# Performance work log

Measured on AMD Instinct MI355X. Metric: run time of the kernel, lower is better.

The kernel has to match this reference:

```python
import jax, jax.numpy as jnp
import numpy as np

NUM_EXPERTS = 8
TOP_K = 2
HIDDEN = 2048
FFN = 4096


def setup_inputs() -> dict:
    key = jax.random.key(0)
    ks = jax.random.split(key, 5)
    s = 0.02
    return {
        "hidden_states": jax.random.normal(ks[0], (2, 2048, HIDDEN), dtype=jnp.float32),
        "w_router": jax.random.normal(ks[1], (HIDDEN, NUM_EXPERTS), dtype=jnp.float32) * s,
        "w1": jax.random.normal(ks[2], (NUM_EXPERTS, FFN, HIDDEN), dtype=jnp.float32) * s,
        "w2": jax.random.normal(ks[3], (NUM_EXPERTS, HIDDEN, FFN), dtype=jnp.float32) * s,
        "w3": jax.random.normal(ks[4], (NUM_EXPERTS, FFN, HIDDEN), dtype=jnp.float32) * s,
    }


def reference(hidden_states, w_router, w1, w2, w3):
    shape = hidden_states.shape
    x = hidden_states.reshape(-1, HIDDEN)  # [T, H]

    # Router: logits -> softmax -> top-k -> renormalize (Mixtral routing)
    logits = x @ w_router                              # [T, E]
    probs = jax.nn.softmax(logits, axis=-1)
    top_w, top_i = jax.lax.top_k(probs, TOP_K)         # [T, K]
    top_w = top_w / jnp.sum(top_w, axis=-1, keepdims=True)
    # Dense combine weights per expert: [T, E]
    combine = jnp.sum(
        jax.nn.one_hot(top_i, NUM_EXPERTS, dtype=x.dtype) * top_w[..., None], axis=1
    )

    # Grouped SwiGLU experts: out = sum_e combine[:, e] * w2_e(silu(w1_e x) * w3_e x)
    out = jnp.zeros_like(x)
    for e in range(NUM_EXPERTS):
        h = jax.nn.silu(x @ w1[e].T) * (x @ w3[e].T)   # [T, F]
        y = h @ w2[e].T                                # [T, H]
        out = out + combine[:, e:e + 1] * y

    return (out.reshape(shape), jnp.zeros((1,), dtype=x.dtype))
```

## Files before the change

### kernel.cpp

```cpp
#include <hip/hip_runtime.h>
#include <hip/hip_bf16.h>
#include <stdint.h>

#define T_TOK 4096
#define HID   2048
#define FFN_D 4096
#define NE    8
#define PADB  256
#define PADMAX 10240

typedef __attribute__((ext_vector_type(8))) short  short8;
typedef __attribute__((ext_vector_type(4))) float  f32x4;
typedef __attribute__((ext_vector_type(4))) unsigned short u16x4;
typedef unsigned short u16;

__device__ __forceinline__ u16 f2bf(float f) {
    unsigned u = __float_as_uint(f);
    u += 0x7FFFu + ((u >> 16) & 1u);
    return (u16)(u >> 16);
}
__device__ __forceinline__ float bf2f(u16 v) {
    return __uint_as_float(((unsigned)v) << 16);
}

#define GLD16(g, l) __builtin_amdgcn_global_load_lds( \
    (const __attribute__((address_space(1))) unsigned int*)(g), \
    (__attribute__((address_space(3))) unsigned int*)(l), 16, 0, 0)

__global__ void k_convert(const float* __restrict__ s, u16* __restrict__ d, long n8) {
    for (long i = (long)blockIdx.x * 256 + threadIdx.x; i < n8; i += (long)gridDim.x * 256) {
        f32x4 a = *((const f32x4*)s + i * 2);
        f32x4 b = *((const f32x4*)s + i * 2 + 1);
        short8 o;
#pragma unroll
        for (int q = 0; q < 4; ++q) { o[q] = (short)f2bf(a[q]); o[q + 4] = (short)f2bf(b[q]); }
        *(short8*)(d + i * 8) = o;
    }
}

__global__ void k_convert2(const float* __restrict__ s0, u16* __restrict__ d0,
                           const float* __restrict__ s1, u16* __restrict__ d1, long n8) {
    for (long i = (long)blockIdx.x * 256 + threadIdx.x; i < 2 * n8; i += (long)gridDim.x * 256) {
        const float* s = (i < n8) ? s0 : s1;
        u16*         d = (i < n8) ? d0 : d1;
        long         j = (i < n8) ? i : (i - n8);
        f32x4 a = *((const f32x4*)s + j * 2);
        f32x4 b = *((const f32x4*)s + j * 2 + 1);
        short8 o;
#pragma unroll
        for (int q = 0; q < 4; ++q) { o[q] = (short)f2bf(a[q]); o[q + 4] = (short)f2bf(b[q]); }
        *(short8*)(d + j * 8) = o;
    }
}

__device__ __forceinline__ void router_body(
    int blk, int tid,
    const float* __restrict__ x, const float* __restrict__ wr,
    u16* __restrict__ xb, int* __restrict__ topk_id,
    float* __restrict__ topk_w, int* __restrict__ counts) {
    int lane = tid & 63;
    int t = blk * 4 + (tid >> 6);
    const float* xr = x + (size_t)t * HID;
    u16* xbr = xb + (size_t)t * HID;
    float acc[8];
#pragma unroll
    for (int e = 0; e < 8; ++e) acc[e] = 0.f;
    for (int h = lane; h < HID; h += 64) {
        float xv = xr[h];
        xbr[h] = f2bf(xv);
        f32x4 w0 = *(const f32x4*)(wr + h * 8);
        f32x4 w1 = *(const f32x4*)(wr + h * 8 + 4);
#pragma unroll
        for (int q = 0; q < 4; ++q) { acc[q] += xv * w0[q]; acc[4 + q] += xv * w1[q]; }
    }
#pragma unroll
    for (int e = 0; e < 8; ++e) {
        float v = acc[e];
#pragma unroll
        for (int s = 32; s > 0; s >>= 1) v += __shfl_xor(v, s);
        acc[e] = v;
    }
    if (lane == 0) {
        int i0 = 0; float l0 = acc[0];
#pragma unroll
        for (int e = 1; e < 8; ++e) if (acc[e] > l0) { l0 = acc[e]; i0 = e; }
        int i1 = -1; float l1 = -3.4e38f;
#pragma unroll
        for (int e = 0; e < 8; ++e) if (e != i0 && acc[e] > l1) { l1 = acc[e]; i1 = e; }
        float wA = 1.f / (1.f + expf(l1 - l0));
        topk_id[t * 2] = i0;  topk_id[t * 2 + 1] = i1;
        topk_w[t * 2] = wA;   topk_w[t * 2 + 1] = 1.f - wA;
        atomicAdd(&counts[i0], 1);
        atomicAdd(&counts[i1], 1);
    }
}

__global__ void k_router(const float* __restrict__ x, const float* __restrict__ wr,
                         u16* __restrict__ xb, int* __restrict__ topk_id,
                         float* __restrict__ topk_w, int* __restrict__ counts) {
    router_body(blockIdx.x, threadIdx.x, x, wr, xb, topk_id, topk_w, counts);
}

__global__ void k_pre(const float* __restrict__ x, const float* __restrict__ wr,
                      u16* __restrict__ xb, int* __restrict__ topk_id,
                      float* __restrict__ topk_w, int* __restrict__ counts,
                      const float* __restrict__ w1, u16* __restrict__ w1b,
                      const float* __restrict__ w3, u16* __restrict__ w3b, long n8) {
    if (blockIdx.x < 1024) {
        router_body(blockIdx.x, threadIdx.x, x, wr, xb, topk_id, topk_w, counts);
        return;
    }
    const long nb = (long)(gridDim.x - 1024);
    for (long i = (long)(blockIdx.x - 1024) * 256 + threadIdx.x; i < 2 * n8; i += nb * 256) {
        const float* s = (i < n8) ? w1 : w3;
        u16*         d = (i < n8) ? w1b : w3b;
        long         j = (i < n8) ? i : (i - n8);
        f32x4 a = *((const f32x4*)s + j * 2);
        f32x4 b = *((const f32x4*)s + j * 2 + 1);
        short8 o;
#pragma unroll
        for (int q = 0; q < 4; ++q) { o[q] = (short)f2bf(a[q]); o[q + 4] = (short)f2bf(b[q]); }
        *(short8*)(d + j * 8) = o;
    }
}

__global__ void k_scan(const int* __restrict__ counts, int* __restrict__ pad_off,
                       int* __restrict__ perm_tok) {
    __shared__ int sTot;
    if (threadIdx.x == 0) {
        int o = 0;
#pragma unroll
        for (int e = 0; e < 8; ++e) { pad_off[e] = o; o += ((counts[e] + PADB - 1) / PADB) * PADB; }
        pad_off[8] = o; sTot = o;
    }
    __syncthreads();
    int tot = sTot;
    for (int i = threadIdx.x; i < tot; i += 256) perm_tok[i] = 0;
}

__global__ void k_scatter(const int* __restrict__ topk_id, int* __restrict__ cursors,
                          const int* __restrict__ pad_off, int* __restrict__ perm_tok,
                          int* __restrict__ pos_of) {
    int t = blockIdx.x * 256 + threadIdx.x;
    if (t >= T_TOK) return;
#pragma unroll
    for (int k = 0; k < 2; ++k) {
        int e = topk_id[t * 2 + k];
        int p = pad_off[e] + atomicAdd(&cursors[e], 1);
        perm_tok[p] = t;
        pos_of[t * 2 + k] = p;
    }
}

template<int KTOT, int NTOT, int BNt, int KSPLIT, bool DUAL, bool GATHER, bool CONV>
__global__ __launch_bounds__(512, 2) void k_gemm8(
    const u16* __restrict__ A,
    const u16* __restrict__ B0all,
    const u16* __restrict__ B1all,
    u16* __restrict__ C,
    const int* __restrict__ perm_tok,
    const int* __restrict__ pad_off,
    const float* __restrict__ W2c,
    u16* __restrict__ W2d,
    int gemmBlk, int convBlk)
{
    constexpr int BMt   = 256;
    constexpr int WCW   = BNt / 4;
    constexpr int NI    = WCW / 16;
    constexpr int CPX   = (NTOT / BNt) / 8;
    constexpr int KPART = KTOT / KSPLIT;
    constexpr int NK    = KPART / 64;
    constexpr int ATILE = BMt * 64;
    constexpr int BTILE = BNt * 64;
    constexpr int SEGB  = DUAL ? 8 : (BNt == 256 ? 8 : 4);

    const int bid = blockIdx.x;
    const int tid = threadIdx.x;

    if (CONV && bid >= gemmBlk) {
        const long per = (long)NE * FFN_D * HID / 8 / convBlk;
        const long i0 = (long)(bid - gemmBlk) * per;
        for (long i = i0 + tid; i < i0 + per; i += 512) {
            f32x4 a = *((const f32x4*)W2c + i * 2);
            f32x4 b = *((const f32x4*)W2c + i * 2 + 1);
            short8 o;
#pragma unroll
            for (int q = 0; q < 4; ++q) { o[q] = (short)f2bf(a[q]); o[q + 4] = (short)f2bf(b[q]); }
            *(short8*)(W2d + i * 8) = o;
        }
        return;
    }

    const int xcd = bid & 7;
    int idx = bid >> 3;
    const int kh  = idx & (KSPLIT - 1);
    idx /= KSPLIT;
    const int m0  = (idx / CPX) * BMt;
    if (m0 >= pad_off[8]) return;
    const int n0  = (xcd * CPX + (idx % CPX)) * BNt;
    int e = 0;
    while (pad_off[e + 1] <= m0) ++e;

    __shared__ u16 As[2 * ATILE];
    __shared__ u16 Bs0[2 * BTILE];
    __shared__ u16 Bs1[DUAL ? 2 * BTILE : 8];
    __shared__ int tokS[GATHER ? BMt : 8];

    const int w = tid >> 6, l = tid & 63;
    if (GATHER) {
        for (int i = tid; i < BMt; i += 512) tokS[i] = perm_tok[m0 + i];
        __syncthreads();
    }

    const u16* B0 = B0all + (size_t)e * NTOT * KTOT;
    const u16* B1 = DUAL ? (B1all + (size_t)e * NTOT * KTOT) : B0all;
    const int k0e = kh * KPART;

    const int nseg = (w < 4) ? 8 : SEGB;
    const u16* gsrc[8];
    u16* ldst[8];
    int tstep;
    {
        const int c = (l & 7) ^ (l >> 3);
#pragma unroll
        for (int j = 0; j < 8; ++j) {
            const int js = (j < nseg) ? j : (j - 4);
            const int rl = js * 8 + (l >> 3);
            if (w < 4) {
                const int rt = w * 64 + rl;
                const long grow = GATHER ? (long)tokS[rt] : (long)(m0 + rt);
                gsrc[j] = A + grow * KTOT + k0e + c * 8;
                ldst[j] = (u16*)As + (w * 64 + js * 8) * 64;
                tstep = ATILE;
            } else if (DUAL && w >= 6) {
                const int rt = (w - 6) * 64 + rl;
                gsrc[j] = B1 + (size_t)(n0 + rt) * KTOT + k0e + c * 8;
                ldst[j] = (u16*)Bs1 + (rt - rl + js * 8) * 64;
                tstep = BTILE;
            } else {
                const int rt = DUAL ? ((w - 4) * 64 + rl)
                                    : (BNt == 256 ? ((w - 4) * 64 + rl)
                                                  : ((w - 4) * 32 + rl));
                gsrc[j] = B0 + (size_t)(n0 + rt) * KTOT + k0e + c * 8;
                ldst[j] = (u16*)Bs0 + (rt - rl + js * 8) * 64;
                tstep = BTILE;
            }
        }
    }

    const int wr = w >> 2, wc = w & 3;
    const int fr = l & 15, fk = l >> 4, x7 = l & 7;
    const int pc0 = ((fk ^ x7) << 3);
    const int pc1 = pc0 ^ 32;
    const int aB = (wr * 128 + fr) * 64;
    const int bB = (wc * WCW + fr) * 64;

    f32x4 acc0[8][NI], acc1[8][NI];
    const f32x4 fz = {0.f, 0.f, 0.f, 0.f};
#pragma unroll
    for (int mi = 0; mi < 8; ++mi)
#pragma unroll
        for (int ni = 0; ni < NI; ++ni) { acc0[mi][ni] = fz; if (DUAL) acc1[mi][ni] = fz; }

#pragma unroll
    for (int j = 0; j < 8; ++j) if (j < nseg) GLD16(gsrc[j], ldst[j]);
    asm volatile("s_waitcnt vmcnt(0)" ::: "memory");
    __builtin_amdgcn_s_barrier();
    __builtin_amdgcn_sched_barrier(0);

#pragma unroll 1
    for (int t = 0; t < NK; ++t) {
        const int cb = t & 1, nb2 = cb ^ 1;
        const u16* aC  = (const u16*)As  + cb * ATILE;
        const u16* b0C = (const u16*)Bs0 + cb * BTILE;
        const u16* b1C = (const u16*)Bs1 + (DUAL ? cb * BTILE : 0);
        const long kE = (long)(t + 1) * 64;
        const bool hasNext = (t + 1 < NK);

        short8 af[4], b0f[NI], b1f[NI];

        if (hasNext) {
#pragma unroll
            for (int j = 0; j < 4; ++j) if (j < nseg) GLD16(gsrc[j] + kE, ldst[j] + nb2 * tstep);
        }
#pragma unroll
        for (int mi = 0; mi < 4; ++mi) af[mi] = *(const short8*)(aC + aB + mi * 1024 + pc0);
#pragma unroll
        for (int ni = 0; ni < NI; ++ni) {
            b0f[ni] = *(const short8*)(b0C + bB + ni * 1024 + pc0);
            if (DUAL) b1f[ni] = *(const short8*)(b1C + bB + ni * 1024 + pc0);
        }
        __builtin_amdgcn_s_setprio(1);
#pragma unroll
        for (int mi = 0; mi < 4; ++mi)
#pragma unroll
            for (int ni = 0; ni < NI; ++ni) {
                acc0[mi][ni] = __builtin_amdgcn_mfma_f32_16x16x32_bf16(af[mi], b0f[ni], acc0[mi][ni], 0, 0, 0);
                if (DUAL)
                    acc1[mi][ni] = __builtin_amdgcn_mfma_f32_16x16x32_bf16(af[mi], b1f[ni], acc1[mi][ni], 0, 0, 0);
            }
        __builtin_amdgcn_s_setprio(0);

        if (hasNext) {
#pragma unroll
            for (int j = 4; j < 8; ++j) if (j < nseg) GLD16(gsrc[j] + kE, ldst[j] + nb2 * tstep);
        }
#pragma unroll
        for (int mi = 0; mi < 4; ++mi) af[mi] = *(const short8*)(aC + aB + (mi + 4) * 1024 + pc0);
        __builtin_amdgcn_s_setprio(1);
#pragma unroll
        for (int mi = 0; mi < 4; ++mi)
#pragma unroll
            for (int ni = 0; ni < NI; ++ni) {
                acc0[mi + 4][ni] = __builtin_amdgcn_mfma_f32_16x16x32_bf16(af[mi], b0f[ni], acc0[mi + 4][ni], 0, 0, 0);
                if (DUAL)
                    acc1[mi + 4][ni] = __builtin_amdgcn_mfma_f32_16x16x32_bf16(af[mi], b1f[ni], acc1[mi + 4][ni], 0, 0, 0);
            }
        __builtin_amdgcn_s_setprio(0);

#pragma unroll
        for (int mi = 0; mi < 4; ++mi) af[mi] = *(const short8*)(aC + aB + mi * 1024 + pc1);
#pragma unroll
        for (int ni = 0; ni < NI; ++ni) {
            b0f[ni] = *(const short8*)(b0C + bB + ni * 1024 + pc1);
            if (DUAL) b1f[ni] = *(const short8*)(b1C + bB + ni * 1024 + pc1);
        }
        __builtin_amdgcn_s_setprio(1);
#pragma unroll
        for (int mi = 0; mi < 4; ++mi)
#pragma unroll
            for (int ni = 0; ni < NI; ++ni) {
                acc0[mi][ni] = __builtin_amdgcn_mfma_f32_16x16x32_bf16(af[mi], b0f[ni], acc0[mi][ni], 0, 0, 0);
                if (DUAL)
                    acc1[mi][ni] = __builtin_amdgcn_mfma_f32_16x16x32_bf16(af[mi], b1f[ni], acc1[mi][ni], 0, 0, 0);
            }
        __builtin_amdgcn_s_setprio(0);

#pragma unroll
        for (int mi = 0; mi < 4; ++mi) af[mi] = *(const short8*)(aC + aB + (mi + 4) * 1024 + pc1);
        __builtin_amdgcn_s_setprio(1);
#pragma unroll
        for (int mi = 0; mi < 4; ++mi)
#pragma unroll
            for (int ni = 0; ni < NI; ++ni) {
                acc0[mi + 4][ni] = __builtin_amdgcn_mfma_f32_16x16x32_bf16(af[mi], b0f[ni], acc0[mi + 4][ni], 0, 0, 0);
                if (DUAL)
                    acc1[mi + 4][ni] = __builtin_amdgcn_mfma_f32_16x16x32_bf16(af[mi], b1f[ni], acc1[mi + 4][ni], 0, 0, 0);
            }
        __builtin_amdgcn_s_setprio(0);

        asm volatile("s_waitcnt vmcnt(0)" ::: "memory");
        __builtin_amdgcn_s_barrier();
        __builtin_amdgcn_sched_barrier(0);
    }

    u16* Co = C + (KSPLIT > 1 ? (size_t)kh * PADMAX * NTOT : 0);
    const int er = (l >> 4) * 4;
    const int ec = l & 15;
#pragma unroll
    for (int mi = 0; mi < 8; ++mi)
#pragma unroll
        for (int ni = 0; ni < NI; ++ni)
#pragma unroll
            for (int r = 0; r < 4; ++r) {
                size_t prow = (size_t)(m0 + wr * 128 + mi * 16 + er + r);
                int col = n0 + wc * WCW + ni * 16 + ec;
                float v = acc0[mi][ni][r];
                float res;
                if (DUAL) {
                    float g3 = acc1[mi][ni][r];
                    res = v / (1.f + __expf(-v)) * g3;
                } else {
                    res = v;
                }
                Co[prow * NTOT + col] = f2bf(res);
            }
}

__global__ void k_combine4(const u16* __restrict__ y, const int* __restrict__ pos_of,
                           const float* __restrict__ topk_w, float* __restrict__ out) {
    int idx = blockIdx.x * 256 + threadIdx.x;
    int t  = idx >> 9;
    int c4 = (idx & 511) << 2;
    int p0 = pos_of[t * 2], p1 = pos_of[t * 2 + 1];
    float w0 = topk_w[t * 2], w1 = topk_w[t * 2 + 1];
    const size_t PS = (size_t)PADMAX * HID;
    f32x4 o = {0.f, 0.f, 0.f, 0.f};
#pragma unroll
    for (int p = 0; p < 4; ++p) {
        u16x4 a = *(const u16x4*)(y + p * PS + (size_t)p0 * HID + c4);
        u16x4 b = *(const u16x4*)(y + p * PS + (size_t)p1 * HID + c4);
#pragma unroll
        for (int q = 0; q < 4; ++q) o[q] += w0 * bf2f(a[q]) + w1 * bf2f(b[q]);
    }
    *(f32x4*)(out + (size_t)t * HID + c4) = o;
    if (idx == 0) out[(size_t)T_TOK * HID] = 0.f;
}

__global__ void k_combine2(const u16* __restrict__ y0, const u16* __restrict__ y1,
                           const int* __restrict__ pos_of,
                           const float* __restrict__ topk_w, float* __restrict__ out) {
    int idx = blockIdx.x * 256 + threadIdx.x;
    int t  = idx >> 9;
    int c4 = (idx & 511) << 2;
    int p0 = pos_of[t * 2], p1 = pos_of[t * 2 + 1];
    float w0 = topk_w[t * 2], w1 = topk_w[t * 2 + 1];
    u16x4 a0 = *(const u16x4*)(y0 + (size_t)p0 * HID + c4);
    u16x4 a1 = *(const u16x4*)(y1 + (size_t)p0 * HID + c4);
    u16x4 b0 = *(const u16x4*)(y0 + (size_t)p1 * HID + c4);
    u16x4 b1 = *(const u16x4*)(y1 + (size_t)p1 * HID + c4);
    f32x4 o;
#pragma unroll
    for (int q = 0; q < 4; ++q)
        o[q] = w0 * (bf2f(a0[q]) + bf2f(a1[q])) + w1 * (bf2f(b0[q]) + bf2f(b1[q]));
    *(f32x4*)(out + (size_t)t * HID + c4) = o;
    if (idx == 0) out[(size_t)T_TOK * HID] = 0.f;
}

__global__ void k_init(int* __restrict__ c) {
    if (threadIdx.x < 16) c[threadIdx.x] = 0;
}

extern "C" void kernel_launch(void* const* d_in, const int* in_sizes, int n_in,
                              void* d_out, int out_size, void* d_ws, size_t ws_size,
                              hipStream_t stream) {
    const float* x  = (const float*)d_in[0];
    const float* wr = (const float*)d_in[1];
    const float* w1 = (const float*)d_in[2];
    const float* w2 = (const float*)d_in[3];
    const float* w3 = (const float*)d_in[4];
    float* out = (float*)d_out;
    char* ws = (char*)d_ws;

    const long WN8 = (long)NE * FFN_D * HID / 8;
    const size_t NEED = 503459840ull;

    if (ws_size >= NEED) {
        u16*  xb  = (u16*)(ws);
        u16*  wA  = (u16*)(ws + 16777216);
        u16*  w3b = (u16*)(ws + 150994944);
        u16*  hb  = (u16*)(ws + 285212672);
        u16*  w2b = (u16*)(ws + 369098752);
        u16*  yb  = (u16*)(ws + 16777216);
        int*  perm_tok = (int*)(ws + 503316480);
        int*  pos_of   = (int*)(ws + 503357440);
        int*  topk_id  = (int*)(ws + 503390208);
        float* topk_w  = (float*)(ws + 503422976);
        int*  cnt      = (int*)(ws + 503455744);
        int*  counts   = cnt;
        int*  cursors  = cnt + 8;
        int*  pad_off  = cnt + 16;

        k_init<<<1, 64, 0, stream>>>(cnt);

        k_pre<<<9216, 256, 0, stream>>>(x, wr, xb, topk_id, topk_w, counts,
                                        w1, wA, w3, w3b, WN8);
        k_scan<<<1, 256, 0, stream>>>(counts, pad_off, perm_tok);
        k_scatter<<<16, 256, 0, stream>>>(topk_id, cursors, pad_off, perm_tok, pos_of);

        k_gemm8<HID, FFN_D, 128, 1, true, true, true>
            <<<(FFN_D / 128) * 40 + 512, 512, 0, stream>>>(
            xb, wA, w3b, hb, perm_tok, pad_off, w2, w2b, (FFN_D / 128) * 40, 512);

        k_gemm8<FFN_D, HID, 256, 4, false, false, false>
            <<<(HID / 256) * 40 * 4, 512, 0, stream>>>(
            hb, w2b, (const u16*)nullptr, yb, perm_tok, pad_off,
            (const float*)nullptr, (u16*)nullptr, 0, 0);

        k_combine4<<<8192, 256, 0, stream>>>(yb, pos_of, topk_w, out);
    } else {
        u16*  xb  = (u16*)(ws);
        u16*  wA  = (u16*)(ws + 16777216);
        u16*  w3b = (u16*)(ws + 150994944);
        u16*  hb  = (u16*)(ws + 285212672);
        u16*  yb  = (u16*)(ws + 150994944);
        int*  perm_tok = (int*)(ws + 369098752);
        int*  pos_of   = (int*)(ws + 369139712);
        int*  topk_id  = (int*)(ws + 369172480);
        float* topk_w  = (float*)(ws + 369205248);
        int*  cnt      = (int*)(ws + 369238016);
        int*  counts   = cnt;
        int*  cursors  = cnt + 8;
        int*  pad_off  = cnt + 16;

        k_init<<<1, 64, 0, stream>>>(cnt);
        k_router<<<1024, 256, 0, stream>>>(x, wr, xb, topk_id, topk_w, counts);
        k_scan<<<1, 256, 0, stream>>>(counts, pad_off, perm_tok);
        k_scatter<<<16, 256, 0, stream>>>(topk_id, cursors, pad_off, perm_tok, pos_of);

        k_convert2<<<8192, 256, 0, stream>>>(w1, wA, w3, w3b, WN8);

        k_gemm8<HID, FFN_D, 128, 1, true, true, false>
            <<<(FFN_D / 128) * 40, 512, 0, stream>>>(
            xb, wA, w3b, hb, perm_tok, pad_off,
            (const float*)nullptr, (u16*)nullptr, 0, 0);

        k_convert<<<4096, 256, 0, stream>>>(w2, wA, WN8);

        k_gemm8<FFN_D, HID, 256, 2, false, false, false>
            <<<(HID / 256) * 40 * 2, 512, 0, stream>>>(
            hb, wA, (const u16*)nullptr, yb, perm_tok, pad_off,
            (const float*)nullptr, (u16*)nullptr, 0, 0);

        k_combine2<<<8192, 256, 0, stream>>>(yb, yb + (size_t)PADMAX * HID,
                                             pos_of, topk_w, out);
    }
}
```

Before: 826.2 us.

## Split LDS tiles into K-half planes with finer-grained load/compute pipelining

Reorganizes the shared-memory tiles into two 32-wide K-half planes per buffer, with a new swizzle and precomputed read offsets. Each half-tile load is issued separately. Partial waits (vmcnt(4)) plus a mid-iteration barrier let the second half of the current tile keep arriving while the first half is being computed. The aim is to hide global-load latency better and overlap copies with MFMA work. In exchange it adds an extra barrier per iteration, and it drops the old special case for the non-dual BNt=128 load layout. If that configuration is used, its B-tile staging may overrun the smaller shared buffer.

Result: slower. 864.8 us, median of 2 (+4.7%).

```diff
diff --git a/kernel.cpp b/kernel.cpp
--- a/kernel.cpp
+++ b/kernel.cpp
@@ -164,15 +164,14 @@
     u16* __restrict__ W2d,
     int gemmBlk, int convBlk)
 {
-    constexpr int BMt   = 256;
-    constexpr int WCW   = BNt / 4;
-    constexpr int NI    = WCW / 16;
-    constexpr int CPX   = (NTOT / BNt) / 8;
-    constexpr int KPART = KTOT / KSPLIT;
-    constexpr int NK    = KPART / 64;
-    constexpr int ATILE = BMt * 64;
-    constexpr int BTILE = BNt * 64;
-    constexpr int SEGB  = DUAL ? 8 : (BNt == 256 ? 8 : 4);
+    constexpr int BMt    = 256;
+    constexpr int WCW    = BNt / 4;
+    constexpr int NI     = WCW / 16;
+    constexpr int CPX    = (NTOT / BNt) / 8;
+    constexpr int KPART  = KTOT / KSPLIT;
+    constexpr int NK     = KPART / 64;
+    constexpr int APLANE = BMt * 32;
+    constexpr int BPLANE = BNt * 32;
 
     const int bid = blockIdx.x;
     const int tid = threadIdx.x;
@@ -201,9 +200,9 @@
     int e = 0;
     while (pad_off[e + 1] <= m0) ++e;
 
-    __shared__ u16 As[2 * ATILE];
-    __shared__ u16 Bs0[2 * BTILE];
-    __shared__ u16 Bs1[DUAL ? 2 * BTILE : 8];
+    __shared__ u16 As[4 * APLANE];
+    __shared__ u16 Bs0[4 * BPLANE];
+    __shared__ u16 Bs1[DUAL ? 4 * BPLANE : 8];
     __shared__ int tokS[GATHER ? BMt : 8];
 
     const int w = tid >> 6, l = tid & 63;
@@ -216,44 +215,34 @@
     const u16* B1 = DUAL ? (B1all + (size_t)e * NTOT * KTOT) : B0all;
     const int k0e = kh * KPART;
 
-    const int nseg = (w < 4) ? 8 : SEGB;
-    const u16* gsrc[8];
-    u16* ldst[8];
-    int tstep;
+    const int csrc = (l & 3) ^ ((l >> 3) & 3);
+    const u16* gsrc[4];
+    u16* ubase;
+    int  plane;
     {
-        const int c = (l & 7) ^ (l >> 3);
-#pragma unroll
-        for (int j = 0; j < 8; ++j) {
-            const int js = (j < nseg) ? j : (j - 4);
-            const int rl = js * 8 + (l >> 3);
-            if (w < 4) {
-                const int rt = w * 64 + rl;
-                const long grow = GATHER ? (long)tokS[rt] : (long)(m0 + rt);
-                gsrc[j] = A + grow * KTOT + k0e + c * 8;
-                ldst[j] = (u16*)As + (w * 64 + js * 8) * 64;
-                tstep = ATILE;
-            } else if (DUAL && w >= 6) {
-                const int rt = (w - 6) * 64 + rl;
-                gsrc[j] = B1 + (size_t)(n0 + rt) * KTOT + k0e + c * 8;
-                ldst[j] = (u16*)Bs1 + (rt - rl + js * 8) * 64;
-                tstep = BTILE;
-            } else {
-                const int rt = DUAL ? ((w - 4) * 64 + rl)
-                                    : (BNt == 256 ? ((w - 4) * 64 + rl)
-                                                  : ((w - 4) * 32 + rl));
-                gsrc[j] = B0 + (size_t)(n0 + rt) * KTOT + k0e + c * 8;
-                ldst[j] = (u16*)Bs0 + (rt - rl + js * 8) * 64;
-                tstep = BTILE;
-            }
+        int R0; u16* Arr; const u16* Mat;
+        if (w < 4)              { R0 = w * 64;       Arr = (u16*)As;  plane = APLANE; Mat = A;  }
+        else if (DUAL && w >= 6){ R0 = (w - 6) * 64; Arr = (u16*)Bs1; plane = BPLANE; Mat = B1; }
+        else                    { R0 = (w - 4) * 64; Arr = (u16*)Bs0; plane = BPLANE; Mat = B0; }
+        ubase = Arr + R0 * 32;
+#pragma unroll
+        for (int j = 0; j < 4; ++j) {
+            const int row = R0 + j * 16 + (l >> 2);
+            long grow;
+            if (w < 4) grow = GATHER ? (long)tokS[row] : (long)(m0 + row);
+            else       grow = (long)(n0 + row);
+            gsrc[j] = Mat + grow * KTOT + k0e + csrc * 8;
         }
     }
 
     const int wr = w >> 2, wc = w & 3;
-    const int fr = l & 15, fk = l >> 4, x7 = l & 7;
-    const int pc0 = ((fk ^ x7) << 3);
-    const int pc1 = pc0 ^ 32;
-    const int aB = (wr * 128 + fr) * 64;
-    const int bB = (wc * WCW + fr) * 64;
+    const int fr = l & 15, fk = l >> 4;
+    const int pcA = (fk ^ ((fr >> 1) & 3)) * 8;
+    int aRd[8], bRd[NI];
+#pragma unroll
+    for (int mi = 0; mi < 8; ++mi) aRd[mi] = (wr * 128 + mi * 16 + fr) * 32 + pcA;
+#pragma unroll
+    for (int ni = 0; ni < NI; ++ni) bRd[ni] = (wc * WCW + ni * 16 + fr) * 32 + pcA;
 
     f32x4 acc0[8][NI], acc1[8][NI];
     const f32x4 fz = {0.f, 0.f, 0.f, 0.f};
@@ -263,32 +252,37 @@
         for (int ni = 0; ni < NI; ++ni) { acc0[mi][ni] = fz; if (DUAL) acc1[mi][ni] = fz; }
 
 #pragma unroll
-    for (int j = 0; j < 8; ++j) if (j < nseg) GLD16(gsrc[j], ldst[j]);
-    asm volatile("s_waitcnt vmcnt(0)" ::: "memory");
+    for (int j = 0; j < 4; ++j) GLD16(gsrc[j],      ubase + 0 * plane + j * 512);
+#pragma unroll
+    for (int j = 0; j < 4; ++j) GLD16(gsrc[j] + 32, ubase + 1 * plane + j * 512);
+    asm volatile("s_waitcnt vmcnt(4)" ::: "memory");
     __builtin_amdgcn_s_barrier();
     __builtin_amdgcn_sched_barrier(0);
 
 #pragma unroll 1
     for (int t = 0; t < NK; ++t) {
-        const int cb = t & 1, nb2 = cb ^ 1;
-        const u16* aC  = (const u16*)As  + cb * ATILE;
-        const u16* b0C = (const u16*)Bs0 + cb * BTILE;
-        const u16* b1C = (const u16*)Bs1 + (DUAL ? cb * BTILE : 0);
-        const long kE = (long)(t + 1) * 64;
+        const int cur = t & 1, nxt = cur ^ 1;
+        const int kE = (t + 1) * 64;
         const bool hasNext = (t + 1 < NK);
+        const u16* aP0  = (const u16*)As  + (cur * 2 + 0) * APLANE;
+        const u16* aP1  = (const u16*)As  + (cur * 2 + 1) * APLANE;
+        const u16* b0P0 = (const u16*)Bs0 + (cur * 2 + 0) * BPLANE;
+        const u16* b0P1 = (const u16*)Bs0 + (cur * 2 + 1) * BPLANE;
+        const u16* b1P0 = (const u16*)Bs1 + (DUAL ? (cur * 2 + 0) * BPLANE : 0);
+        const u16* b1P1 = (const u16*)Bs1 + (DUAL ? (cur * 2 + 1) * BPLANE : 0);
 
         short8 af[4], b0f[NI], b1f[NI];
 
         if (hasNext) {
 #pragma unroll
-            for (int j = 0; j < 4; ++j) if (j < nseg) GLD16(gsrc[j] + kE, ldst[j] + nb2 * tstep);
-        }
-#pragma unroll
-        for (int mi = 0; mi < 4; ++mi) af[mi] = *(const short8*)(aC + aB + mi * 1024 + pc0);
+            for (int j = 0; j < 4; ++j) GLD16(gsrc[j] + kE, ubase + (nxt * 2 + 0) * plane + j * 512);
+        }
+#pragma unroll
+        for (int mi = 0; mi < 4; ++mi) af[mi] = *(const short8*)(aP0 + aRd[mi]);
 #pragma unroll
         for (int ni = 0; ni < NI; ++ni) {
-            b0f[ni] = *(const short8*)(b0C + bB + ni * 1024 + pc0);
-            if (DUAL) b1f[ni] = *(const short8*)(b1C + bB + ni * 1024 + pc0);
+            b0f[ni] = *(const short8*)(b0P0 + bRd[ni]);
+            if (DUAL) b1f[ni] = *(const short8*)(b1P0 + bRd[ni]);
         }
         __builtin_amdgcn_s_setprio(1);
 #pragma unroll
@@ -301,12 +295,8 @@
             }
         __builtin_amdgcn_s_setprio(0);
 
-        if (hasNext) {
-#pragma unroll
-            for (int j = 4; j < 8; ++j) if (j < nseg) GLD16(gsrc[j] + kE, ldst[j] + nb2 * tstep);
-        }
-#pragma unroll
-        for (int mi = 0; mi < 4; ++mi) af[mi] = *(const short8*)(aC + aB + (mi + 4) * 1024 + pc0);
+#pragma unroll
+        for (int mi = 0; mi < 4; ++mi) af[mi] = *(const short8*)(aP0 + aRd[mi + 4]);
         __builtin_amdgcn_s_setprio(1);
 #pragma unroll
         for (int mi = 0; mi < 4; ++mi)
@@ -318,12 +308,21 @@
             }
         __builtin_amdgcn_s_setprio(0);
 
-#pragma unroll
-        for (int mi = 0; mi < 4; ++mi) af[mi] = *(const short8*)(aC + aB + mi * 1024 + pc1);
+        if (hasNext) asm volatile("s_waitcnt vmcnt(4)" ::: "memory");
+        else         asm volatile("s_waitcnt vmcnt(0)" ::: "memory");
+        __builtin_amdgcn_s_barrier();
+        __builtin_amdgcn_sched_barrier(0);
+
+        if (hasNext) {
+#pragma unroll
+            for (int j = 0; j < 4; ++j) GLD16(gsrc[j] + kE + 32, ubase + (nxt * 2 + 1) * plane + j * 512);
+        }
+#pragma unroll
+        for (int mi = 0; mi < 4; ++mi) af[mi] = *(const short8*)(aP1 + aRd[mi]);
 #pragma unroll
         for (int ni = 0; ni < NI; ++ni) {
-            b0f[ni] = *(const short8*)(b0C + bB + ni * 1024 + pc1);
-            if (DUAL) b1f[ni] = *(const short8*)(b1C + bB + ni * 1024 + pc1);
+            b0f[ni] = *(const short8*)(b0P1 + bRd[ni]);
+            if (DUAL) b1f[ni] = *(const short8*)(b1P1 + bRd[ni]);
         }
         __builtin_amdgcn_s_setprio(1);
 #pragma unroll
@@ -337,7 +336,7 @@
         __builtin_amdgcn_s_setprio(0);
 
 #pragma unroll
-        for (int mi = 0; mi < 4; ++mi) af[mi] = *(const short8*)(aC + aB + (mi + 4) * 1024 + pc1);
+        for (int mi = 0; mi < 4; ++mi) af[mi] = *(const short8*)(aP1 + aRd[mi + 4]);
         __builtin_amdgcn_s_setprio(1);
 #pragma unroll
         for (int mi = 0; mi < 4; ++mi)
@@ -349,9 +348,11 @@
             }
         __builtin_amdgcn_s_setprio(0);
 
-        asm volatile("s_waitcnt vmcnt(0)" ::: "memory");
-        __builtin_amdgcn_s_barrier();
-        __builtin_amdgcn_sched_barrier(0);
+        if (hasNext) {
+            asm volatile("s_waitcnt vmcnt(4)" ::: "memory");
+            __builtin_amdgcn_s_barrier();
+            __builtin_amdgcn_sched_barrier(0);
+        }
     }
 
     u16* Co = C + (KSPLIT > 1 ? (size_t)kh * PADMAX * NTOT : 0);
```
